# Kernel optimization log

Hardware: AMD Instinct MI355X
Metric: run time of the kernel (lower is better)

Reference implementation:

```python
import jax, jax.numpy as jnp
import numpy as np

N_NODES = 100000
N_EDGES = 1600000
N_GRAPHS = 256
IN_C = 64
HID = 64


def _gcn_conv(x, W, b, src, dst, w, n):
    # GCNConv: x' = D^{-1/2} (A + I) D^{-1/2} (x W) + b, with edge weights w
    x = x @ W
    deg = jnp.zeros((n,), x.dtype).at[dst].add(w) + 1.0  # +1 for self-loop weight
    dinv = jax.lax.rsqrt(deg)
    norm = dinv[src] * w * dinv[dst]                      # [E]
    agg = jnp.zeros_like(x).at[dst].add(x[src] * norm[:, None])
    agg = agg + x * (1.0 / deg)[:, None]                  # self-loop term: d^{-1/2}*1*d^{-1/2}
    return agg + b


def setup_inputs() -> dict:
    key = jax.random.key(0)
    ks = jax.random.split(key, 16)
    inp = {
        "x": jax.random.normal(ks[0], (N_NODES, IN_C), jnp.float32),
        "edge_index": jax.random.randint(ks[1], (2, N_EDGES), 0, N_NODES, jnp.int32),
        "edge_weight": jax.random.uniform(ks[2], (N_EDGES,), jnp.float32),
        "batch": jnp.sort(jax.random.randint(ks[3], (N_NODES,), 0, N_GRAPHS, jnp.int32)),
    }
    s = 0.05
    inp["W0"] = jax.random.normal(ks[4], (IN_C, HID), jnp.float32) * s
    inp["b0"] = jnp.zeros((HID,), jnp.float32)
    inp["W1"] = jax.random.normal(ks[5], (HID, HID), jnp.float32) * s
    inp["b1"] = jnp.zeros((HID,), jnp.float32)
    inp["W2"] = jax.random.normal(ks[6], (HID, HID), jnp.float32) * s
    inp["b2"] = jnp.zeros((HID,), jnp.float32)
    inp["Wr0"] = jax.random.normal(ks[7], (HID, HID // 2), jnp.float32) * s
    inp["br0"] = jnp.zeros((HID // 2,), jnp.float32)
    inp["Wr1"] = jax.random.normal(ks[8], (HID // 2, 1), jnp.float32) * s
    inp["br1"] = jnp.zeros((1,), jnp.float32)
    return inp


def reference(x, edge_index, edge_weight, batch, W0, b0, W1, b1, W2, b2, Wr0, br0, Wr1, br1):
    n = x.shape[0]
    src, dst = edge_index[0], edge_index[1]
    h = jax.nn.relu(_gcn_conv(x, W0, b0, src, dst, edge_weight, n))
    h = jax.nn.relu(_gcn_conv(h, W1, b1, src, dst, edge_weight, n))
    h = _gcn_conv(h, W2, b2, src, dst, edge_weight, n)  # no activation on last GNN layer
    # MLP readout: hidden -> hidden//2 -> 1
    h = jax.nn.relu(h @ Wr0 + br0) @ Wr1 + br1          # [N, 1]
    # scatter-mean pooling by graph id
    sums = jax.ops.segment_sum(h, batch, num_segments=N_GRAPHS)
    cnt = jax.ops.segment_sum(jnp.ones((n, 1), h.dtype), batch, num_segments=N_GRAPHS)
    return sums / jnp.maximum(cnt, 1.0)
```

## Files before the change

### kernel.cpp

```cpp
#include <hip/hip_runtime.h>


#define NBK 391

__device__ __forceinline__ float bcastf(float v, int l) {
    return __int_as_float(__builtin_amdgcn_readlane(__float_as_int(v), l));
}

__global__ void hist_kernel(const int* __restrict__ dst,
                            int* __restrict__ bcnt, int ne) {
    __shared__ int h[512];
    for (int i = threadIdx.x; i < 512; i += blockDim.x) h[i] = 0;
    __syncthreads();
    int stride = gridDim.x * blockDim.x;
    for (int e = blockIdx.x * blockDim.x + threadIdx.x; e < ne; e += stride)
        atomicAdd(&h[dst[e] >> 8], 1);
    __syncthreads();
    for (int i = threadIdx.x; i < 512; i += blockDim.x)
        if (h[i]) atomicAdd(&bcnt[i], h[i]);
}

__global__ void bscan_kernel(const int* __restrict__ bcnt,
                             int* __restrict__ bbase,
                             int* __restrict__ gcur, int nb, int ne) {
    __shared__ int sh[512];
    int t = threadIdx.x;
    int v = (t < nb) ? bcnt[t] : 0;
    sh[t] = v;
    __syncthreads();
    for (int off = 1; off < 512; off <<= 1) {
        int u = (t >= off) ? sh[t - off] : 0;
        __syncthreads();
        sh[t] += u;
        __syncthreads();
    }
    if (t < nb) {
        int e = sh[t] - v;
        bbase[t] = e;
        gcur[t] = e;
    }
    if (t == 0) bbase[nb] = ne;
}

__global__ void scatterB_kernel(const int* __restrict__ src,
                                const int* __restrict__ dst,
                                const float* __restrict__ ew,
                                int* __restrict__ gcur,
                                int2* __restrict__ packed, int ne) {
    __shared__ int h[512];
    __shared__ int cur[512];
    int chunk = (ne + gridDim.x - 1) / gridDim.x;
    int e0 = blockIdx.x * chunk;
    int e1 = e0 + chunk; if (e1 > ne) e1 = ne;
    for (int i = threadIdx.x; i < 512; i += blockDim.x) h[i] = 0;
    __syncthreads();
    for (int e = e0 + threadIdx.x; e < e1; e += blockDim.x)
        atomicAdd(&h[dst[e] >> 8], 1);
    __syncthreads();
    for (int i = threadIdx.x; i < 512; i += blockDim.x)
        cur[i] = h[i] ? atomicAdd(&gcur[i], h[i]) : 0;
    __syncthreads();
    for (int e = e0 + threadIdx.x; e < e1; e += blockDim.x) {
        int d = dst[e];
        int pos = atomicAdd(&cur[d >> 8], 1);
        int2 v;
        v.x = ((d & 255) << 24) | src[e];
        v.y = __float_as_int(ew[e]);
        packed[pos] = v;
    }
}

__global__ void bucket_build_kernel(const int2* __restrict__ packed,
                                    const int* __restrict__ bbase,
                                    int* __restrict__ rptr,
                                    int* __restrict__ cnt,
                                    float* __restrict__ dinv,
                                    int2* __restrict__ csr, int n) {
    __shared__ int cl[256];
    __shared__ int sc[256];
    __shared__ int cur[256];
    int b = blockIdx.x;
    int t = threadIdx.x;
    int node0 = b << 8;
    int nn = n - node0; if (nn > 256) nn = 256;
    int ebase = bbase[b];
    int m = bbase[b + 1] - ebase;
    cl[t] = 0;
    __syncthreads();
    for (int j = t; j < m; j += 256) {
        int local = ((unsigned)packed[ebase + j].x) >> 24;
        atomicAdd(&cl[local], 1);
    }
    __syncthreads();
    int c = cl[t];
    sc[t] = c;
    __syncthreads();
    for (int off = 1; off < 256; off <<= 1) {
        int u = (t >= off) ? sc[t - off] : 0;
        __syncthreads();
        sc[t] += u;
        __syncthreads();
    }
    int base = ebase + sc[t] - c;
    cur[t] = base;
    if (t < nn) {
        rptr[node0 + t] = base;
        cnt[node0 + t] = c;
    }
    __syncthreads();
    for (int j = t; j < m; j += 256) {
        int2 p = packed[ebase + j];
        int local = ((unsigned)p.x) >> 24;
        int pos = atomicAdd(&cur[local], 1);
        int2 v;
        v.x = p.x & 0x00FFFFFF;
        v.y = p.y;
        csr[pos] = v;
    }
    __syncthreads();
    if (t < nn) {
        float s = 0.0f;
        for (int j = base; j < base + c; ++j)
            s += __int_as_float(csr[j].y);
        dinv[node0 + t] = 1.0f / sqrtf(s + 1.0f);
    }
}

template <bool RELU>
__global__ void __launch_bounds__(256, 4)
gemm_rl_kernel(const float* __restrict__ X, const float* W,
               const float* __restrict__ dinv, float* __restrict__ Ts,
               int n) {
    __shared__ float Wl[4096];
    {
        const float4* Wv = (const float4*)W;
        float4* Lv = (float4*)Wl;
        for (int i = threadIdx.x; i < 1024; i += 256) Lv[i] = Wv[i];
    }
    __syncthreads();
    int lane = threadIdx.x & 63;
    int wid  = (blockIdx.x * blockDim.x + threadIdx.x) >> 6;
    int nw   = (gridDim.x * blockDim.x) >> 6;
    int lrow = lane >> 4;
    int lcol = (lane & 15) * 4;
    for (int r0 = wid * 4; r0 + 4 <= n; r0 += nw * 4) {
        float4 xv = *(const float4*)&X[(size_t)(r0 + lrow) * 64 + lcol];
        if (RELU) {
            xv.x = fmaxf(xv.x, 0.f); xv.y = fmaxf(xv.y, 0.f);
            xv.z = fmaxf(xv.z, 0.f); xv.w = fmaxf(xv.w, 0.f);
        }
        float a0 = 0.f, a1 = 0.f, a2 = 0.f, a3 = 0.f;
#pragma unroll
        for (int k4 = 0; k4 < 16; ++k4) {
            float w0 = Wl[(4 * k4 + 0) * 64 + lane];
            float w1 = Wl[(4 * k4 + 1) * 64 + lane];
            float w2 = Wl[(4 * k4 + 2) * 64 + lane];
            float w3 = Wl[(4 * k4 + 3) * 64 + lane];
            a0 = fmaf(bcastf(xv.x, k4), w0, a0);
            a0 = fmaf(bcastf(xv.y, k4), w1, a0);
            a0 = fmaf(bcastf(xv.z, k4), w2, a0);
            a0 = fmaf(bcastf(xv.w, k4), w3, a0);
            a1 = fmaf(bcastf(xv.x, 16 + k4), w0, a1);
            a1 = fmaf(bcastf(xv.y, 16 + k4), w1, a1);
            a1 = fmaf(bcastf(xv.z, 16 + k4), w2, a1);
            a1 = fmaf(bcastf(xv.w, 16 + k4), w3, a1);
            a2 = fmaf(bcastf(xv.x, 32 + k4), w0, a2);
            a2 = fmaf(bcastf(xv.y, 32 + k4), w1, a2);
            a2 = fmaf(bcastf(xv.z, 32 + k4), w2, a2);
            a2 = fmaf(bcastf(xv.w, 32 + k4), w3, a2);
            a3 = fmaf(bcastf(xv.x, 48 + k4), w0, a3);
            a3 = fmaf(bcastf(xv.y, 48 + k4), w1, a3);
            a3 = fmaf(bcastf(xv.z, 48 + k4), w2, a3);
            a3 = fmaf(bcastf(xv.w, 48 + k4), w3, a3);
        }
        Ts[(size_t)(r0 + 0) * 64 + lane] = a0 * dinv[r0 + 0];
        Ts[(size_t)(r0 + 1) * 64 + lane] = a1 * dinv[r0 + 1];
        Ts[(size_t)(r0 + 2) * 64 + lane] = a2 * dinv[r0 + 2];
        Ts[(size_t)(r0 + 3) * 64 + lane] = a3 * dinv[r0 + 3];
    }
    if (wid == 0) {
        for (int r = (n & ~3); r < n; ++r) {
            const float4* xr = (const float4*)(X + (size_t)r * 64);
            float acc = 0.f;
#pragma unroll
            for (int k4 = 0; k4 < 16; ++k4) {
                float4 a = xr[k4];
                if (RELU) {
                    a.x = fmaxf(a.x, 0.f); a.y = fmaxf(a.y, 0.f);
                    a.z = fmaxf(a.z, 0.f); a.w = fmaxf(a.w, 0.f);
                }
                acc = fmaf(a.x, Wl[(4 * k4 + 0) * 64 + lane], acc);
                acc = fmaf(a.y, Wl[(4 * k4 + 1) * 64 + lane], acc);
                acc = fmaf(a.z, Wl[(4 * k4 + 2) * 64 + lane], acc);
                acc = fmaf(a.w, Wl[(4 * k4 + 3) * 64 + lane], acc);
            }
            Ts[(size_t)r * 64 + lane] = acc * dinv[r];
        }
    }
}

__global__ void __launch_bounds__(256, 4)
fgather_kernel(const int2* __restrict__ csr,
               const int* __restrict__ rptr,
               const int* __restrict__ cnt,
               const float* __restrict__ dinv,
               const float* __restrict__ b,
               const float* __restrict__ Ts_in,
               const float* Wn,
               float* __restrict__ Ts_out, int n) {
    __shared__ float Wl[4096];
    {
        const float4* Wv = (const float4*)Wn;
        float4* Lv = (float4*)Wl;
        for (int i = threadIdx.x; i < 1024; i += 256) Lv[i] = Wv[i];
    }
    __syncthreads();
    int lane = threadIdx.x & 63;
    int r = (int)(((size_t)blockIdx.x * blockDim.x + threadIdx.x) >> 6);
    if (r >= n) return;
    int sub = lane >> 4;
    int cl  = lane & 15;
    int start = rptr[r];
    int m = cnt[r];
    float4 a0 = {0.f, 0.f, 0.f, 0.f};
    float4 a1 = {0.f, 0.f, 0.f, 0.f};
    float4 a2 = {0.f, 0.f, 0.f, 0.f};
    float4 a3 = {0.f, 0.f, 0.f, 0.f};
    int j = sub;
    for (; j + 12 < m; j += 16) {
        int2 e0 = csr[start + j];
        int2 e1 = csr[start + j + 4];
        int2 e2 = csr[start + j + 8];
        int2 e3 = csr[start + j + 12];
        float w0 = __int_as_float(e0.y);
        float w1 = __int_as_float(e1.y);
        float w2 = __int_as_float(e2.y);
        float w3 = __int_as_float(e3.y);
        float4 t0 = *(const float4*)&Ts_in[(size_t)e0.x * 64 + cl * 4];
        float4 t1 = *(const float4*)&Ts_in[(size_t)e1.x * 64 + cl * 4];
        float4 t2 = *(const float4*)&Ts_in[(size_t)e2.x * 64 + cl * 4];
        float4 t3 = *(const float4*)&Ts_in[(size_t)e3.x * 64 + cl * 4];
        a0.x = fmaf(t0.x, w0, a0.x); a0.y = fmaf(t0.y, w0, a0.y);
        a0.z = fmaf(t0.z, w0, a0.z); a0.w = fmaf(t0.w, w0, a0.w);
        a1.x = fmaf(t1.x, w1, a1.x); a1.y = fmaf(t1.y, w1, a1.y);
        a1.z = fmaf(t1.z, w1, a1.z); a1.w = fmaf(t1.w, w1, a1.w);
        a2.x = fmaf(t2.x, w2, a2.x); a2.y = fmaf(t2.y, w2, a2.y);
        a2.z = fmaf(t2.z, w2, a2.z); a2.w = fmaf(t2.w, w2, a2.w);
        a3.x = fmaf(t3.x, w3, a3.x); a3.y = fmaf(t3.y, w3, a3.y);
        a3.z = fmaf(t3.z, w3, a3.z); a3.w = fmaf(t3.w, w3, a3.w);
    }
    for (; j < m; j += 4) {
        int2 e0 = csr[start + j];
        float w0 = __int_as_float(e0.y);
        float4 t0 = *(const float4*)&Ts_in[(size_t)e0.x * 64 + cl * 4];
        a0.x = fmaf(t0.x, w0, a0.x); a0.y = fmaf(t0.y, w0, a0.y);
        a0.z = fmaf(t0.z, w0, a0.z); a0.w = fmaf(t0.w, w0, a0.w);
    }
    a0.x += a1.x + a2.x + a3.x;
    a0.y += a1.y + a2.y + a3.y;
    a0.z += a1.z + a2.z + a3.z;
    a0.w += a1.w + a2.w + a3.w;
#pragma unroll
    for (int off = 16; off < 64; off <<= 1) {
        a0.x += __shfl_xor(a0.x, off);
        a0.y += __shfl_xor(a0.y, off);
        a0.z += __shfl_xor(a0.z, off);
        a0.w += __shfl_xor(a0.w, off);
    }
    float dv = dinv[r];
    float4 ts = *(const float4*)&Ts_in[(size_t)r * 64 + cl * 4];
    float4 bb = *(const float4*)&b[cl * 4];
    float tx = fmaxf(fmaf(dv, a0.x + ts.x, bb.x), 0.f);
    float ty = fmaxf(fmaf(dv, a0.y + ts.y, bb.y), 0.f);
    float tz = fmaxf(fmaf(dv, a0.z + ts.z, bb.z), 0.f);
    float tw = fmaxf(fmaf(dv, a0.w + ts.w, bb.w), 0.f);
    float acc = 0.f;
#pragma unroll
    for (int q = 0; q < 16; ++q) {
        acc = fmaf(bcastf(tx, q), Wl[(4 * q + 0) * 64 + lane], acc);
        acc = fmaf(bcastf(ty, q), Wl[(4 * q + 1) * 64 + lane], acc);
        acc = fmaf(bcastf(tz, q), Wl[(4 * q + 2) * 64 + lane], acc);
        acc = fmaf(bcastf(tw, q), Wl[(4 * q + 3) * 64 + lane], acc);
    }
    Ts_out[(size_t)r * 64 + lane] = acc * dv;
}

__global__ void gather_kernel(const int2* __restrict__ csr,
                              const int* __restrict__ rptr,
                              const int* __restrict__ cnt,
                              const float* __restrict__ dinv,
                              const float* __restrict__ b,
                              const float* __restrict__ Ts,
                              float* __restrict__ A, int n) {
    int lane = threadIdx.x & 63;
    int r = (int)(((size_t)blockIdx.x * blockDim.x + threadIdx.x) >> 6);
    if (r >= n) return;
    int sub = lane >> 4;
    int cl  = lane & 15;
    int start = rptr[r];
    int m = cnt[r];
    float4 a0 = {0.f, 0.f, 0.f, 0.f};
    float4 a1 = {0.f, 0.f, 0.f, 0.f};
    float4 a2 = {0.f, 0.f, 0.f, 0.f};
    float4 a3 = {0.f, 0.f, 0.f, 0.f};
    int j = sub;
    for (; j + 12 < m; j += 16) {
        int2 e0 = csr[start + j];
        int2 e1 = csr[start + j + 4];
        int2 e2 = csr[start + j + 8];
        int2 e3 = csr[start + j + 12];
        float w0 = __int_as_float(e0.y);
        float w1 = __int_as_float(e1.y);
        float w2 = __int_as_float(e2.y);
        float w3 = __int_as_float(e3.y);
        float4 t0 = *(const float4*)&Ts[(size_t)e0.x * 64 + cl * 4];
        float4 t1 = *(const float4*)&Ts[(size_t)e1.x * 64 + cl * 4];
        float4 t2 = *(const float4*)&Ts[(size_t)e2.x * 64 + cl * 4];
        float4 t3 = *(const float4*)&Ts[(size_t)e3.x * 64 + cl * 4];
        a0.x = fmaf(t0.x, w0, a0.x); a0.y = fmaf(t0.y, w0, a0.y);
        a0.z = fmaf(t0.z, w0, a0.z); a0.w = fmaf(t0.w, w0, a0.w);
        a1.x = fmaf(t1.x, w1, a1.x); a1.y = fmaf(t1.y, w1, a1.y);
        a1.z = fmaf(t1.z, w1, a1.z); a1.w = fmaf(t1.w, w1, a1.w);
        a2.x = fmaf(t2.x, w2, a2.x); a2.y = fmaf(t2.y, w2, a2.y);
        a2.z = fmaf(t2.z, w2, a2.z); a2.w = fmaf(t2.w, w2, a2.w);
        a3.x = fmaf(t3.x, w3, a3.x); a3.y = fmaf(t3.y, w3, a3.y);
        a3.z = fmaf(t3.z, w3, a3.z); a3.w = fmaf(t3.w, w3, a3.w);
    }
    for (; j < m; j += 4) {
        int2 e0 = csr[start + j];
        float w0 = __int_as_float(e0.y);
        float4 t0 = *(const float4*)&Ts[(size_t)e0.x * 64 + cl * 4];
        a0.x = fmaf(t0.x, w0, a0.x); a0.y = fmaf(t0.y, w0, a0.y);
        a0.z = fmaf(t0.z, w0, a0.z); a0.w = fmaf(t0.w, w0, a0.w);
    }
    a0.x += a1.x + a2.x + a3.x;
    a0.y += a1.y + a2.y + a3.y;
    a0.z += a1.z + a2.z + a3.z;
    a0.w += a1.w + a2.w + a3.w;
#pragma unroll
    for (int off = 16; off < 64; off <<= 1) {
        a0.x += __shfl_xor(a0.x, off);
        a0.y += __shfl_xor(a0.y, off);
        a0.z += __shfl_xor(a0.z, off);
        a0.w += __shfl_xor(a0.w, off);
    }
    if (sub == 0) {
        float dv = dinv[r];
        float4 ts = *(const float4*)&Ts[(size_t)r * 64 + cl * 4];
        float4 bb = *(const float4*)&b[cl * 4];
        float4 o;
        o.x = fmaf(dv, a0.x + ts.x, bb.x);
        o.y = fmaf(dv, a0.y + ts.y, bb.y);
        o.z = fmaf(dv, a0.z + ts.z, bb.z);
        o.w = fmaf(dv, a0.w + ts.w, bb.w);
        *(float4*)&A[(size_t)r * 64 + cl * 4] = o;
    }
}

__global__ void readout_kernel(const float* __restrict__ H,
                               const float* __restrict__ Wr0,
                               const float* __restrict__ br0,
                               const float* __restrict__ Wr1,
                               const float* __restrict__ br1,
                               const int* __restrict__ batch,
                               float* __restrict__ gsum,
                               float* __restrict__ gcnt, int n) {
    __shared__ float Ws[64 * 32];
    __shared__ float w1s[32];
    for (int i = threadIdx.x; i < 64 * 32; i += blockDim.x) Ws[i] = Wr0[i];
    if (threadIdx.x < 32) w1s[threadIdx.x] = Wr1[threadIdx.x];
    __syncthreads();
    int r = blockIdx.x * blockDim.x + threadIdx.x;
    int lane = threadIdx.x & 63;
    float sv = 0.0f;
    int g = -1;
    if (r < n) {
        float h[64];
        const float4* hr = (const float4*)(H + (size_t)r * 64);
#pragma unroll
        for (int i = 0; i < 16; ++i) {
            float4 v = hr[i];
            h[4 * i + 0] = v.x; h[4 * i + 1] = v.y;
            h[4 * i + 2] = v.z; h[4 * i + 3] = v.w;
        }
        float ssum = 0.0f;
#pragma unroll 1
        for (int jg = 0; jg < 8; ++jg) {
            float a0 = br0[jg * 4 + 0], a1 = br0[jg * 4 + 1];
            float a2 = br0[jg * 4 + 2], a3 = br0[jg * 4 + 3];
#pragma unroll
            for (int k = 0; k < 64; ++k) {
                const float4 wv = *(const float4*)&Ws[k * 32 + jg * 4];
                a0 = fmaf(h[k], wv.x, a0);
                a1 = fmaf(h[k], wv.y, a1);
                a2 = fmaf(h[k], wv.z, a2);
                a3 = fmaf(h[k], wv.w, a3);
            }
            a0 = fmaxf(a0, 0.0f); a1 = fmaxf(a1, 0.0f);
            a2 = fmaxf(a2, 0.0f); a3 = fmaxf(a3, 0.0f);
            ssum += a0 * w1s[jg * 4 + 0] + a1 * w1s[jg * 4 + 1] +
                    a2 * w1s[jg * 4 + 2] + a3 * w1s[jg * 4 + 3];
        }
        sv = ssum + br1[0];
        g = batch[r];
    }
    float c = (r < n) ? 1.0f : 0.0f;
#pragma unroll
    for (int off = 1; off < 64; off <<= 1) {
        int   og = __shfl_down(g, off);
        float ov = __shfl_down(sv, off);
        float oc = __shfl_down(c, off);
        if ((lane + off) < 64 && og == g) { sv += ov; c += oc; }
    }
    int gprev = __shfl_up(g, 1);
    bool head = (lane == 0) || (gprev != g);
    if (head && g >= 0) {
        atomicAdd(&gsum[g], sv);
        atomicAdd(&gcnt[g], c);
    }
}

__global__ void pool_fin_kernel(const float* __restrict__ gsum,
                                const float* __restrict__ gcnt,
                                float* __restrict__ out, int ng) {
    int g = blockIdx.x * blockDim.x + threadIdx.x;
    if (g < ng) out[g] = gsum[g] / fmaxf(gcnt[g], 1.0f);
}

extern "C" void kernel_launch(void* const* d_in, const int* in_sizes, int n_in,
                              void* d_out, int out_size, void* d_ws, size_t ws_size,
                              hipStream_t stream) {
    const float* x    = (const float*)d_in[0];
    const int*   ei   = (const int*)d_in[1];
    const float* ew   = (const float*)d_in[2];
    const int*   batch= (const int*)d_in[3];
    const float* W0   = (const float*)d_in[4];
    const float* b0   = (const float*)d_in[5];
    const float* W1   = (const float*)d_in[6];
    const float* b1   = (const float*)d_in[7];
    const float* W2   = (const float*)d_in[8];
    const float* b2   = (const float*)d_in[9];
    const float* Wr0  = (const float*)d_in[10];
    const float* br0  = (const float*)d_in[11];
    const float* Wr1  = (const float*)d_in[12];
    const float* br1  = (const float*)d_in[13];
    float* out = (float*)d_out;

    int n  = in_sizes[0] / 64;
    int ne = in_sizes[1] / 2;
    int ng = out_size;
    const int* srcv = ei;
    const int* dstv = ei + ne;
    int nbk = (n + 255) >> 8;

    char* ws = (char*)d_ws;
    size_t off = 0;
    auto alloc = [&](size_t bytes) {
        void* p = ws + off;
        off += (bytes + 255) & ~(size_t)255;
        return p;
    };
    float* Ts     = (float*)alloc((size_t)n * 64 * sizeof(float));
    float* A      = (float*)alloc((size_t)n * 64 * sizeof(float));
    float* dinv   = (float*)alloc((size_t)n * sizeof(float));
    int*   cnt    = (int*)alloc((size_t)n * sizeof(int));
    int*   rptr   = (int*)alloc((size_t)n * sizeof(int));
    int*   bcnt   = (int*)alloc(520 * sizeof(int));
    int*   bbase  = (int*)alloc(520 * sizeof(int));
    int*   gcur   = (int*)alloc(520 * sizeof(int));
    int2*  csr    = (int2*)alloc((size_t)ne * sizeof(int2));
    float* gsum   = (float*)alloc((size_t)ng * sizeof(float));
    float* gcnt   = (float*)alloc((size_t)ng * sizeof(float));
    int2*  packed = (int2*)Ts;
    (void)ws_size;

    hipMemsetAsync(bcnt, 0, 520 * sizeof(int), stream);
    hipMemsetAsync(gsum, 0, (size_t)ng * sizeof(float), stream);
    hipMemsetAsync(gcnt, 0, (size_t)ng * sizeof(float), stream);

    hist_kernel<<<256, 256, 0, stream>>>(dstv, bcnt, ne);
    bscan_kernel<<<1, 512, 0, stream>>>(bcnt, bbase, gcur, nbk, ne);
    scatterB_kernel<<<200, 256, 0, stream>>>(srcv, dstv, ew, gcur, packed, ne);
    bucket_build_kernel<<<nbk, 256, 0, stream>>>(packed, bbase, rptr, cnt,
                                                 dinv, csr, n);

    const int gemm_blocks = 2048;
    unsigned gat_blocks = (unsigned)(((size_t)n * 64 + 255) / 256);

    gemm_rl_kernel<false><<<gemm_blocks, 256, 0, stream>>>(x, W0, dinv, Ts, n);
    fgather_kernel<<<gat_blocks, 256, 0, stream>>>(csr, rptr, cnt, dinv, b0,
                                                   Ts, W1, A, n);
    fgather_kernel<<<gat_blocks, 256, 0, stream>>>(csr, rptr, cnt, dinv, b1,
                                                   A, W2, Ts, n);
    gather_kernel<<<gat_blocks, 256, 0, stream>>>(csr, rptr, cnt, dinv, b2,
                                                  Ts, A, n);

    readout_kernel<<<(n + 255) / 256, 256, 0, stream>>>(A, Wr0, br0, Wr1, br1,
                                                        batch, gsum, gcnt, n);
    pool_fin_kernel<<<(ng + 255) / 256, 256, 0, stream>>>(gsum, gcnt, out, ng);
}
```

Measured before the change: 359.7 us.

## Fuse last-layer gather with MLP readout and split pooling into its own kernel

The final GCN gather now computes the MLP readout (64→32 ReLU, then 32→1) directly from the aggregated row held in registers, using wavefront lane broadcasts and LDS-resident weights. It writes one scalar per node instead of the full 64-wide hidden matrix, so the separate readout kernel no longer has to re-read it. Pooling moves into a light segpool kernel. The fgather matvec also splits its single accumulator into four independent chains to shorten the FMA dependency chain. The cost is extra LDS weight loading per block and a __launch_bounds__ constraint on the fused kernel.

```diff
diff --git a/kernel.cpp b/kernel.cpp
--- a/kernel.cpp
+++ b/kernel.cpp
@@ -274,24 +274,40 @@
     float ty = fmaxf(fmaf(dv, a0.y + ts.y, bb.y), 0.f);
     float tz = fmaxf(fmaf(dv, a0.z + ts.z, bb.z), 0.f);
     float tw = fmaxf(fmaf(dv, a0.w + ts.w, bb.w), 0.f);
-    float acc = 0.f;
+    float c0 = 0.f, c1 = 0.f, c2 = 0.f, c3 = 0.f;
 #pragma unroll
     for (int q = 0; q < 16; ++q) {
-        acc = fmaf(bcastf(tx, q), Wl[(4 * q + 0) * 64 + lane], acc);
-        acc = fmaf(bcastf(ty, q), Wl[(4 * q + 1) * 64 + lane], acc);
-        acc = fmaf(bcastf(tz, q), Wl[(4 * q + 2) * 64 + lane], acc);
-        acc = fmaf(bcastf(tw, q), Wl[(4 * q + 3) * 64 + lane], acc);
-    }
-    Ts_out[(size_t)r * 64 + lane] = acc * dv;
-}
-
-__global__ void gather_kernel(const int2* __restrict__ csr,
-                              const int* __restrict__ rptr,
-                              const int* __restrict__ cnt,
-                              const float* __restrict__ dinv,
-                              const float* __restrict__ b,
-                              const float* __restrict__ Ts,
-                              float* __restrict__ A, int n) {
+        c0 = fmaf(bcastf(tx, q), Wl[(4 * q + 0) * 64 + lane], c0);
+        c1 = fmaf(bcastf(ty, q), Wl[(4 * q + 1) * 64 + lane], c1);
+        c2 = fmaf(bcastf(tz, q), Wl[(4 * q + 2) * 64 + lane], c2);
+        c3 = fmaf(bcastf(tw, q), Wl[(4 * q + 3) * 64 + lane], c3);
+    }
+    Ts_out[(size_t)r * 64 + lane] = ((c0 + c1) + (c2 + c3)) * dv;
+}
+
+__global__ void __launch_bounds__(256, 4)
+rgather_kernel(const int2* __restrict__ csr,
+               const int* __restrict__ rptr,
+               const int* __restrict__ cnt,
+               const float* __restrict__ dinv,
+               const float* __restrict__ b,
+               const float* __restrict__ Ts,
+               const float* Wr0, const float* br0,
+               const float* Wr1, const float* br1,
+               float* __restrict__ svbuf, int n) {
+    __shared__ float Wl[64 * 32];
+    __shared__ float w1s[32];
+    __shared__ float b0s[32];
+    {
+        const float4* Wv = (const float4*)Wr0;
+        float4* Lv = (float4*)Wl;
+        for (int i = threadIdx.x; i < 512; i += 256) Lv[i] = Wv[i];
+        if (threadIdx.x < 32) {
+            w1s[threadIdx.x] = Wr1[threadIdx.x];
+            b0s[threadIdx.x] = br0[threadIdx.x];
+        }
+    }
+    __syncthreads();
     int lane = threadIdx.x & 63;
     int r = (int)(((size_t)blockIdx.x * blockDim.x + threadIdx.x) >> 6);
     if (r >= n) return;
@@ -344,66 +360,38 @@
         a0.z += __shfl_xor(a0.z, off);
         a0.w += __shfl_xor(a0.w, off);
     }
-    if (sub == 0) {
-        float dv = dinv[r];
-        float4 ts = *(const float4*)&Ts[(size_t)r * 64 + cl * 4];
-        float4 bb = *(const float4*)&b[cl * 4];
-        float4 o;
-        o.x = fmaf(dv, a0.x + ts.x, bb.x);
-        o.y = fmaf(dv, a0.y + ts.y, bb.y);
-        o.z = fmaf(dv, a0.z + ts.z, bb.z);
-        o.w = fmaf(dv, a0.w + ts.w, bb.w);
-        *(float4*)&A[(size_t)r * 64 + cl * 4] = o;
-    }
-}
-
-__global__ void readout_kernel(const float* __restrict__ H,
-                               const float* __restrict__ Wr0,
-                               const float* __restrict__ br0,
-                               const float* __restrict__ Wr1,
-                               const float* __restrict__ br1,
+    float dv = dinv[r];
+    float4 ts = *(const float4*)&Ts[(size_t)r * 64 + cl * 4];
+    float4 bb = *(const float4*)&b[cl * 4];
+    float tx = fmaf(dv, a0.x + ts.x, bb.x);
+    float ty = fmaf(dv, a0.y + ts.y, bb.y);
+    float tz = fmaf(dv, a0.z + ts.z, bb.z);
+    float tw = fmaf(dv, a0.w + ts.w, bb.w);
+    int hj = lane & 31;
+    float c0 = 0.f, c1 = 0.f, c2 = 0.f, c3 = 0.f;
+#pragma unroll
+    for (int q = 0; q < 16; ++q) {
+        c0 = fmaf(bcastf(tx, q), Wl[(4 * q + 0) * 32 + hj], c0);
+        c1 = fmaf(bcastf(ty, q), Wl[(4 * q + 1) * 32 + hj], c1);
+        c2 = fmaf(bcastf(tz, q), Wl[(4 * q + 2) * 32 + hj], c2);
+        c3 = fmaf(bcastf(tw, q), Wl[(4 * q + 3) * 32 + hj], c3);
+    }
+    float h = fmaxf(((c0 + c1) + (c2 + c3)) + b0s[hj], 0.f);
+    float p = h * w1s[hj];
+#pragma unroll
+    for (int off = 1; off < 32; off <<= 1) p += __shfl_xor(p, off);
+    if (lane == 0) svbuf[r] = p + br1[0];
+}
+
+__global__ void segpool_kernel(const float* __restrict__ svbuf,
                                const int* __restrict__ batch,
                                float* __restrict__ gsum,
                                float* __restrict__ gcnt, int n) {
-    __shared__ float Ws[64 * 32];
-    __shared__ float w1s[32];
-    for (int i = threadIdx.x; i < 64 * 32; i += blockDim.x) Ws[i] = Wr0[i];
-    if (threadIdx.x < 32) w1s[threadIdx.x] = Wr1[threadIdx.x];
-    __syncthreads();
     int r = blockIdx.x * blockDim.x + threadIdx.x;
     int lane = threadIdx.x & 63;
     float sv = 0.0f;
     int g = -1;
-    if (r < n) {
-        float h[64];
-        const float4* hr = (const float4*)(H + (size_t)r * 64);
-#pragma unroll
-        for (int i = 0; i < 16; ++i) {
-            float4 v = hr[i];
-            h[4 * i + 0] = v.x; h[4 * i + 1] = v.y;
-            h[4 * i + 2] = v.z; h[4 * i + 3] = v.w;
-        }
-        float ssum = 0.0f;
-#pragma unroll 1
-        for (int jg = 0; jg < 8; ++jg) {
-            float a0 = br0[jg * 4 + 0], a1 = br0[jg * 4 + 1];
-            float a2 = br0[jg * 4 + 2], a3 = br0[jg * 4 + 3];
-#pragma unroll
-            for (int k = 0; k < 64; ++k) {
-                const float4 wv = *(const float4*)&Ws[k * 32 + jg * 4];
-                a0 = fmaf(h[k], wv.x, a0);
-                a1 = fmaf(h[k], wv.y, a1);
-                a2 = fmaf(h[k], wv.z, a2);
-                a3 = fmaf(h[k], wv.w, a3);
-            }
-            a0 = fmaxf(a0, 0.0f); a1 = fmaxf(a1, 0.0f);
-            a2 = fmaxf(a2, 0.0f); a3 = fmaxf(a3, 0.0f);
-            ssum += a0 * w1s[jg * 4 + 0] + a1 * w1s[jg * 4 + 1] +
-                    a2 * w1s[jg * 4 + 2] + a3 * w1s[jg * 4 + 3];
-        }
-        sv = ssum + br1[0];
-        g = batch[r];
-    }
+    if (r < n) { sv = svbuf[r]; g = batch[r]; }
     float c = (r < n) ? 1.0f : 0.0f;
 #pragma unroll
     for (int off = 1; off < 64; off <<= 1) {
@@ -463,6 +451,7 @@
     float* Ts     = (float*)alloc((size_t)n * 64 * sizeof(float));
     float* A      = (float*)alloc((size_t)n * 64 * sizeof(float));
     float* dinv   = (float*)alloc((size_t)n * sizeof(float));
+    float* svbuf  = (float*)alloc((size_t)n * sizeof(float));
     int*   cnt    = (int*)alloc((size_t)n * sizeof(int));
     int*   rptr   = (int*)alloc((size_t)n * sizeof(int));
     int*   bcnt   = (int*)alloc(520 * sizeof(int));
@@ -492,10 +481,10 @@
                                                    Ts, W1, A, n);
     fgather_kernel<<<gat_blocks, 256, 0, stream>>>(csr, rptr, cnt, dinv, b1,
                                                    A, W2, Ts, n);
-    gather_kernel<<<gat_blocks, 256, 0, stream>>>(csr, rptr, cnt, dinv, b2,
-                                                  Ts, A, n);
-
-    readout_kernel<<<(n + 255) / 256, 256, 0, stream>>>(A, Wr0, br0, Wr1, br1,
-                                                        batch, gsum, gcnt, n);
+    rgather_kernel<<<gat_blocks, 256, 0, stream>>>(csr, rptr, cnt, dinv, b2,
+                                                   Ts, Wr0, br0, Wr1, br1,
+                                                   svbuf, n);
+    segpool_kernel<<<(n + 255) / 256, 256, 0, stream>>>(svbuf, batch,
+                                                        gsum, gcnt, n);
     pool_fin_kernel<<<(ng + 255) / 256, 256, 0, stream>>>(gsum, gcnt, out, ng);
 }
```

Measured after the change: 355.9 us. Within noise of the previous version (-1.0%).
